# Performance work log

Hardware: AMD Instinct MI355X
Metric: run time of the kernel (lower is better)

## Reference

```python
import jax, jax.numpy as jnp
import numpy as np

T = 100          # sequence length (number of GRU steps)
H = 50           # carry/hidden dim
Z = 10           # latent dim
OUT = Z + Z * (Z + 1) // 2  # 65: mean + tril Cholesky entries
LN_EPS = 1e-6    # flax LayerNorm default epsilon


def setup_inputs() -> dict:
    key = jax.random.key(0)
    ks = jax.random.split(key, 8)
    # Orthogonal-ish recurrent kernels via QR for well-conditioned dynamics
    def ortho(k):
        a = jax.random.normal(k, (H, H), dtype=jnp.float32)
        q, _ = jnp.linalg.qr(a)
        return q
    return {
        "carry_init": jax.random.normal(ks[0], (H,), dtype=jnp.float32),
        "W_hr": ortho(ks[1]), "b_hr": jnp.zeros((H,), jnp.float32),
        "s_r": jnp.ones((H,), jnp.float32), "o_r": jnp.zeros((H,), jnp.float32),
        "W_hz": ortho(ks[2]), "b_hz": jnp.zeros((H,), jnp.float32),
        "s_z": jnp.ones((H,), jnp.float32), "o_z": jnp.zeros((H,), jnp.float32),
        "W_hn": ortho(ks[3]), "b_hn": jnp.zeros((H,), jnp.float32),
        "s_n": jnp.ones((H,), jnp.float32), "o_n": jnp.zeros((H,), jnp.float32),
        "W_dense": jax.random.normal(ks[4], (H, OUT), jnp.float32) * (1.0 / jnp.sqrt(H)),
        "b_dense": jnp.zeros((OUT,), jnp.float32),
    }


def _layernorm(x, scale, bias):
    mu = jnp.mean(x, axis=-1, keepdims=True)
    var = jnp.mean(jnp.square(x - mu), axis=-1, keepdims=True)
    return (x - mu) * jax.lax.rsqrt(var + LN_EPS) * scale + bias


def reference(carry_init, W_hr, b_hr, s_r, o_r, W_hz, b_hz, s_z, o_z,
              W_hn, b_hn, s_n, o_n, W_dense, b_dense):
    # Input to the GRU is zeros((T,1)) -> cell ignores it entirely (no input kernel).
    def step(h, _):
        r = jax.nn.sigmoid(_layernorm(h @ W_hr + b_hr, s_r, o_r))
        z = jax.nn.sigmoid(_layernorm(h @ W_hz + b_hz, s_z, o_z))
        n = jnp.tanh(r * _layernorm(h @ W_hn + b_hn, s_n, o_n))
        new_h = (1.0 - z) * n + z * h
        return new_h, new_h

    _, hs = jax.lax.scan(step, carry_init, None, length=T)  # (T, H)
    out = hs @ W_dense + b_dense                              # (T, OUT)

    tril = jnp.tril_indices(Z)
    eye = jnp.eye(Z, dtype=out.dtype)

    def nat(x):
        mu, flat = x[:Z], x[Z:]
        L = jnp.zeros((Z, Z), dtype=x.dtype).at[tril].set(flat)
        d = jax.nn.softplus(jnp.diagonal(L))  # positive diagonal -> PD Sigma
        L = L.at[jnp.diag_indices(Z)].set(d)
        Sigma = L @ L.T
        # psd_solve: J = Sigma^{-1} via Cholesky solve
        J = jax.scipy.linalg.cho_solve((L, True), eye)
        h_nat = J @ mu
        return Sigma, mu, J, h_nat

    Sigma, mu, J, h_nat = jax.vmap(nat)(out)
    return Sigma, mu, J, h_nat
```

## Files before the change

### kernel.cpp

```cpp
#include <hip/hip_runtime.h>
#include <hip/hip_bf16.h>
#include <math.h>

#define T_STEPS 100
#define H_DIM   50
#define Z_DIM   10
#define OUT_DIM 65
#define KP      25

typedef _Float16 half2v __attribute__((ext_vector_type(2)));

__device__ __forceinline__ float bcast_lane(float v, int lane) {
    return __uint_as_float(__builtin_amdgcn_readlane(__float_as_uint(v), lane));
}
__device__ __forceinline__ unsigned readlane_u(unsigned v, int lane) {
    return (unsigned)__builtin_amdgcn_readlane((int)v, lane);
}
template<int CTRL>
__device__ __forceinline__ float dpp_mov(float x) {
    return __uint_as_float((unsigned)__builtin_amdgcn_update_dpp(
        0, (int)__float_as_uint(x), CTRL, 0xF, 0xF, true));
}
#define DPP_ROW_SHL1 0x101
#define DPP_SHR1     0x111
#define DPP_SHR2     0x112
#define DPP_SHR4     0x114
#define DPP_SHR8     0x118
#define DPP_BCAST15  0x142
#define DPP_BCAST31  0x143

__device__ __forceinline__ unsigned pack_h2(float lo, float hi) {
#if __has_builtin(__builtin_amdgcn_cvt_pkrtz)
    return __builtin_bit_cast(unsigned, __builtin_amdgcn_cvt_pkrtz(lo, hi));
#else
    half2v p; p.x = (_Float16)lo; p.y = (_Float16)hi;
    return __builtin_bit_cast(unsigned, p);
#endif
}
__device__ __forceinline__ float fdot2h(unsigned a, unsigned b, float c) {
#if __has_builtin(__builtin_amdgcn_fdot2)
    return __builtin_amdgcn_fdot2(__builtin_bit_cast(half2v, a),
                                  __builtin_bit_cast(half2v, b), c, false);
#else
    const half2v x = __builtin_bit_cast(half2v, a);
    const half2v y = __builtin_bit_cast(half2v, b);
    return fmaf((float)x.x, (float)y.x, fmaf((float)x.y, (float)y.y, c));
#endif
}

__device__ __forceinline__ float fast_rcp(float x) { return __builtin_amdgcn_rcpf(x); }
__device__ __forceinline__ float fast_rsq(float x) { return __builtin_amdgcn_rsqf(x); }
__device__ __forceinline__ float fast_sigmoid(float x) {
    return fast_rcp(1.0f + __expf(-x));
}
__device__ __forceinline__ float fast_tanh(float y) {
    return 1.0f - 2.0f * fast_rcp(__expf(2.0f * y) + 1.0f);
}

__global__ __launch_bounds__(192, 1)
void gru_recur_kernel(
    const float* __restrict__ carry_init,
    const float* __restrict__ W_hr, const float* __restrict__ b_hr,
    const float* __restrict__ s_r,  const float* __restrict__ o_r,
    const float* __restrict__ W_hz, const float* __restrict__ b_hz,
    const float* __restrict__ s_z,  const float* __restrict__ o_z,
    const float* __restrict__ W_hn, const float* __restrict__ b_hn,
    const float* __restrict__ s_n,  const float* __restrict__ o_n,
    float* __restrict__ ws_h)
{
    const int  tid   = threadIdx.x;
    const int  wave  = tid >> 6;
    const int  j     = tid & 63;
    const bool valid = (j < H_DIM);
    const int  jc    = valid ? j : 0;

    const float* Wg = (wave == 0) ? W_hr : (wave == 1) ? W_hz : W_hn;
    const float* bg = (wave == 0) ? b_hr : (wave == 1) ? b_hz : b_hn;
    const float* sg = (wave == 0) ? s_r  : (wave == 1) ? s_z  : s_n;
    const float* og = (wave == 0) ? o_r  : (wave == 1) ? o_z  : o_n;

    unsigned w[KP];
    #pragma unroll
    for (int k = 0; k < KP; ++k) {
        const int i0 = 2 * k, i1 = 2 * k + 1;
        w[k] = pack_h2(valid ? Wg[i0 * H_DIM + j] : 0.0f,
                       valid ? Wg[i1 * H_DIM + j] : 0.0f);
    }
    #pragma unroll
    for (int k = 0; k < KP; ++k) asm volatile("" : "+v"(w[k]));

    const float bj = valid ? bg[jc] : 0.0f;
    const float sc = sg[jc];
    const float of = og[jc];

    __shared__ float gbuf[2][3][64];
    __shared__ __align__(16) float hist[T_STEPS][64];

    float h = valid ? carry_init[jc] : 0.0f;
    const float invH = 1.0f / (float)H_DIM;

    float    hsl = dpp_mov<DPP_ROW_SHL1>(h);
    unsigned hpk = pack_h2(h, hsl);

    #pragma unroll 1
    for (int t = 0; t < T_STEPS; ++t) {
        float a0 = bj, a1 = 0.0f;
        #pragma unroll
        for (int k = 0; k < KP; k += 2) {
            const unsigned s0 = readlane_u(hpk, 2 * k);
            a0 = fdot2h(s0, w[k], a0);
            if (k + 1 < KP) {
                const unsigned s1 = readlane_u(hpk, 2 * (k + 1));
                a1 = fdot2h(s1, w[k + 1], a1);
            }
        }
        const float a = a0 + a1;

        float m = a, q = a * a;
        #define STAGE(C) m += dpp_mov<C>(m); q += dpp_mov<C>(q);
        STAGE(DPP_SHR1) STAGE(DPP_SHR2) STAGE(DPP_SHR4)
        STAGE(DPP_SHR8) STAGE(DPP_BCAST15) STAGE(DPP_BCAST31)
        #undef STAGE
        m = bcast_lane(m, 63); q = bcast_lane(q, 63);

        const float mu  = m * invH;
        const float var = fmaxf(q * invH - mu * mu, 0.0f);
        const float g   = (a - mu) * fast_rsq(var + 1e-6f) * sc + of;
        const float val = (wave == 2) ? g : fast_sigmoid(g);

        gbuf[t & 1][wave][j] = val;
        __syncthreads();

        const float r  = gbuf[t & 1][0][j];
        const float z  = gbuf[t & 1][1][j];
        const float gn = gbuf[t & 1][2][j];
        const float n  = fast_tanh(r * gn);
        h = n + z * (h - n);

        if (wave == 0) hist[t][j] = h;

        hsl = dpp_mov<DPP_ROW_SHL1>(h);
        hpk = pack_h2(h, hsl);
    }

    __syncthreads();
    {
        float4*       dst = (float4*)ws_h;
        const float4* src = (const float4*)hist;
        for (int i = tid; i < T_STEPS * 16; i += 192)
            dst[i] = src[i];
    }
}

__global__ __launch_bounds__(128)
void dense_nat_kernel(
    const float* __restrict__ W_dense, const float* __restrict__ b_dense,
    const float* __restrict__ ws_h, float* __restrict__ out)
{
    const int t   = blockIdx.x;
    const int tid = threadIdx.x;

    __shared__ float hloc[H_DIM];
    __shared__ float dl  [OUT_DIM];
    __shared__ float Lp  [55];
    __shared__ float Li  [55];
    __shared__ float Jsh [100];

    if (tid < H_DIM) hloc[tid] = ws_h[t * 64 + tid];
    __syncthreads();

    if (tid < OUT_DIM) {
        float acc = b_dense[tid];
        #pragma unroll
        for (int i = 0; i < H_DIM; ++i)
            acc = fmaf(hloc[i], W_dense[i * OUT_DIM + tid], acc);
        dl[tid] = acc;
    }
    __syncthreads();

    if (tid < 55) {
        float v = dl[Z_DIM + tid];
        const bool isd = (tid==0)|(tid==2)|(tid==5)|(tid==9)|(tid==14)|
                         (tid==20)|(tid==27)|(tid==35)|(tid==44)|(tid==54);
        if (isd) v = (v > 20.0f) ? v : log1pf(__expf(v));
        Lp[tid] = v;
    }
    __syncthreads();

    float* outSigma = out;
    float* outMu    = out + 10000;
    float* outJ     = out + 11000;
    float* outHnat  = out + 21000;

    int a = 0;
    {
        #pragma unroll
        for (int x = 1; x < Z_DIM; ++x)
            if (tid >= x * (x + 1) / 2) a = x;
    }
    const int b = tid - a * (a + 1) / 2;

    if (tid < 55) {
        float s = 0.0f;
        for (int k = 0; k <= b; ++k)
            s = fmaf(Lp[a * (a + 1) / 2 + k], Lp[b * (b + 1) / 2 + k], s);
        outSigma[t * 100 + a * 10 + b] = s;
        outSigma[t * 100 + b * 10 + a] = s;
    }
    if (tid >= 64 && tid < 64 + Z_DIM) outMu[t * 10 + (tid - 64)] = dl[tid - 64];
    __syncthreads();

    if (tid < Z_DIM) {
        const int k = tid;
        float dinv[Z_DIM];
        #pragma unroll
        for (int i = 0; i < Z_DIM; ++i)
            dinv[i] = 1.0f / Lp[i * (i + 1) / 2 + i];
        float col[Z_DIM];
        #pragma unroll
        for (int i = 0; i < Z_DIM; ++i) col[i] = 0.0f;
        #pragma unroll
        for (int i = 0; i < Z_DIM; ++i) {
            float s = 0.0f;
            #pragma unroll
            for (int m = 0; m < i; ++m)
                s = fmaf(Lp[i * (i + 1) / 2 + m], col[m], s);
            if (i >= k) col[i] = (i == k) ? dinv[i] : -s * dinv[i];
        }
        #pragma unroll
        for (int i = 0; i < Z_DIM; ++i)
            if (i >= k) Li[i * (i + 1) / 2 + k] = col[i];
    }
    __syncthreads();

    if (tid < 55) {
        float s = 0.0f;
        for (int m = a; m < Z_DIM; ++m)
            s = fmaf(Li[m * (m + 1) / 2 + a], Li[m * (m + 1) / 2 + b], s);
        outJ[t * 100 + a * 10 + b] = s;
        outJ[t * 100 + b * 10 + a] = s;
        Jsh[a * 10 + b] = s;
        Jsh[b * 10 + a] = s;
    }
    __syncthreads();

    if (tid < Z_DIM) {
        float s = 0.0f;
        #pragma unroll
        for (int k = 0; k < Z_DIM; ++k)
            s = fmaf(Jsh[tid * 10 + k], dl[k], s);
        outHnat[t * 10 + tid] = s;
    }
}

extern "C" void kernel_launch(void* const* d_in, const int* in_sizes, int n_in,
                              void* d_out, int out_size, void* d_ws, size_t ws_size,
                              hipStream_t stream) {
    const float* p[15];
    for (int i = 0; i < 15; ++i) p[i] = (const float*)d_in[i];
    float* ws_h = (float*)d_ws;

    gru_recur_kernel<<<dim3(1), dim3(192), 0, stream>>>(
        p[0],
        p[1], p[2], p[3], p[4],
        p[5], p[6], p[7], p[8],
        p[9], p[10], p[11], p[12],
        ws_h);

    dense_nat_kernel<<<dim3(T_STEPS), dim3(128), 0, stream>>>(
        p[13], p[14], ws_h, (float*)d_out);
}
```

Before: 128.4 us.

## Fuse dense/natural-param stage into GRU kernel with pipelined consumer waves

Merges the recurrence and the per-timestep dense projection plus Cholesky inverse into one single-block kernel. Two extra waves process timestep t-1 while the three GRU waves compute step t, alternating timesteps between them and reading hidden states directly from shared memory. This removes the second kernel launch and the workspace round trip, hiding the post-processing behind the serial recurrence. In exchange, every step's block barrier now includes two more waves, and their work can delay the critical path if it exceeds two step durations.

Result: slower. 446.6 us (+247.7%).

```diff
diff --git a/kernel.cpp b/kernel.cpp
--- a/kernel.cpp
+++ b/kernel.cpp
@@ -57,8 +57,12 @@
     return 1.0f - 2.0f * fast_rcp(__expf(2.0f * y) + 1.0f);
 }
 
-__global__ __launch_bounds__(192, 1)
-void gru_recur_kernel(
+__device__ __forceinline__ void lds_fence_wave() {
+    asm volatile("s_waitcnt lgkmcnt(0)" ::: "memory");
+}
+
+__global__ __launch_bounds__(320, 1)
+void gru_fused_kernel(
     const float* __restrict__ carry_init,
     const float* __restrict__ W_hr, const float* __restrict__ b_hr,
     const float* __restrict__ s_r,  const float* __restrict__ o_r,
@@ -66,190 +70,195 @@
     const float* __restrict__ s_z,  const float* __restrict__ o_z,
     const float* __restrict__ W_hn, const float* __restrict__ b_hn,
     const float* __restrict__ s_n,  const float* __restrict__ o_n,
-    float* __restrict__ ws_h)
+    const float* __restrict__ W_dense, const float* __restrict__ b_dense,
+    float* __restrict__ out)
 {
-    const int  tid   = threadIdx.x;
-    const int  wave  = tid >> 6;
-    const int  j     = tid & 63;
-    const bool valid = (j < H_DIM);
-    const int  jc    = valid ? j : 0;
-
-    const float* Wg = (wave == 0) ? W_hr : (wave == 1) ? W_hz : W_hn;
-    const float* bg = (wave == 0) ? b_hr : (wave == 1) ? b_hz : b_hn;
-    const float* sg = (wave == 0) ? s_r  : (wave == 1) ? s_z  : s_n;
-    const float* og = (wave == 0) ? o_r  : (wave == 1) ? o_z  : o_n;
-
-    unsigned w[KP];
-    #pragma unroll
-    for (int k = 0; k < KP; ++k) {
-        const int i0 = 2 * k, i1 = 2 * k + 1;
-        w[k] = pack_h2(valid ? Wg[i0 * H_DIM + j] : 0.0f,
-                       valid ? Wg[i1 * H_DIM + j] : 0.0f);
-    }
-    #pragma unroll
-    for (int k = 0; k < KP; ++k) asm volatile("" : "+v"(w[k]));
-
-    const float bj = valid ? bg[jc] : 0.0f;
-    const float sc = sg[jc];
-    const float of = og[jc];
+    const int tid  = threadIdx.x;
+    const int wave = tid >> 6;
+    const int j    = tid & 63;
 
     __shared__ float gbuf[2][3][64];
     __shared__ __align__(16) float hist[T_STEPS][64];
-
-    float h = valid ? carry_init[jc] : 0.0f;
-    const float invH = 1.0f / (float)H_DIM;
-
-    float    hsl = dpp_mov<DPP_ROW_SHL1>(h);
-    unsigned hpk = pack_h2(h, hsl);
-
-    #pragma unroll 1
-    for (int t = 0; t < T_STEPS; ++t) {
-        float a0 = bj, a1 = 0.0f;
+    __shared__ float Lp[2][56];
+    __shared__ float Li[2][56];
+    __shared__ float Jsh[2][100];
+    __shared__ float mrow[2][12];
+
+    if (wave < 3) {
+        const bool valid = (j < H_DIM);
+        const int  jc    = valid ? j : 0;
+
+        const float* Wg = (wave == 0) ? W_hr : (wave == 1) ? W_hz : W_hn;
+        const float* bg = (wave == 0) ? b_hr : (wave == 1) ? b_hz : b_hn;
+        const float* sg = (wave == 0) ? s_r  : (wave == 1) ? s_z  : s_n;
+        const float* og = (wave == 0) ? o_r  : (wave == 1) ? o_z  : o_n;
+
+        unsigned w[KP];
         #pragma unroll
-        for (int k = 0; k < KP; k += 2) {
-            const unsigned s0 = readlane_u(hpk, 2 * k);
-            a0 = fdot2h(s0, w[k], a0);
-            if (k + 1 < KP) {
-                const unsigned s1 = readlane_u(hpk, 2 * (k + 1));
-                a1 = fdot2h(s1, w[k + 1], a1);
-            }
+        for (int k = 0; k < KP; ++k) {
+            const int i0 = 2 * k, i1 = 2 * k + 1;
+            w[k] = pack_h2(valid ? Wg[i0 * H_DIM + j] : 0.0f,
+                           valid ? Wg[i1 * H_DIM + j] : 0.0f);
         }
-        const float a = a0 + a1;
-
-        float m = a, q = a * a;
-        #define STAGE(C) m += dpp_mov<C>(m); q += dpp_mov<C>(q);
-        STAGE(DPP_SHR1) STAGE(DPP_SHR2) STAGE(DPP_SHR4)
-        STAGE(DPP_SHR8) STAGE(DPP_BCAST15) STAGE(DPP_BCAST31)
-        #undef STAGE
-        m = bcast_lane(m, 63); q = bcast_lane(q, 63);
-
-        const float mu  = m * invH;
-        const float var = fmaxf(q * invH - mu * mu, 0.0f);
-        const float g   = (a - mu) * fast_rsq(var + 1e-6f) * sc + of;
-        const float val = (wave == 2) ? g : fast_sigmoid(g);
-
-        gbuf[t & 1][wave][j] = val;
+        #pragma unroll
+        for (int k = 0; k < KP; ++k) asm volatile("" : "+v"(w[k]));
+
+        const float bj = valid ? bg[jc] : 0.0f;
+        const float sc = sg[jc];
+        const float of = og[jc];
+
+        float h = valid ? carry_init[jc] : 0.0f;
+        const float invH = 1.0f / (float)H_DIM;
+
+        float    hsl = dpp_mov<DPP_ROW_SHL1>(h);
+        unsigned hpk = pack_h2(h, hsl);
+
+        #pragma unroll 1
+        for (int t = 0; t < T_STEPS; ++t) {
+            float a0 = bj, a1 = 0.0f;
+            #pragma unroll
+            for (int k = 0; k < KP; k += 2) {
+                const unsigned s0 = readlane_u(hpk, 2 * k);
+                a0 = fdot2h(s0, w[k], a0);
+                if (k + 1 < KP) {
+                    const unsigned s1 = readlane_u(hpk, 2 * (k + 1));
+                    a1 = fdot2h(s1, w[k + 1], a1);
+                }
+            }
+            const float a = a0 + a1;
+
+            float m = a, q = a * a;
+            #define STAGE(C) m += dpp_mov<C>(m); q += dpp_mov<C>(q);
+            STAGE(DPP_SHR1) STAGE(DPP_SHR2) STAGE(DPP_SHR4)
+            STAGE(DPP_SHR8) STAGE(DPP_BCAST15) STAGE(DPP_BCAST31)
+            #undef STAGE
+            m = bcast_lane(m, 63); q = bcast_lane(q, 63);
+
+            const float mu  = m * invH;
+            const float var = fmaxf(q * invH - mu * mu, 0.0f);
+            const float g   = (a - mu) * fast_rsq(var + 1e-6f) * sc + of;
+            const float val = (wave == 2) ? g : fast_sigmoid(g);
+
+            gbuf[t & 1][wave][j] = val;
+            __syncthreads();
+
+            const float r  = gbuf[t & 1][0][j];
+            const float z  = gbuf[t & 1][1][j];
+            const float gn = gbuf[t & 1][2][j];
+            const float n  = fast_tanh(r * gn);
+            h = n + z * (h - n);
+
+            if (wave == 0) hist[t][j] = h;
+
+            hsl = dpp_mov<DPP_ROW_SHL1>(h);
+            hpk = pack_h2(h, hsl);
+        }
         __syncthreads();
-
-        const float r  = gbuf[t & 1][0][j];
-        const float z  = gbuf[t & 1][1][j];
-        const float gn = gbuf[t & 1][2][j];
-        const float n  = fast_tanh(r * gn);
-        h = n + z * (h - n);
-
-        if (wave == 0) hist[t][j] = h;
-
-        hsl = dpp_mov<DPP_ROW_SHL1>(h);
-        hpk = pack_h2(h, hsl);
-    }
-
-    __syncthreads();
-    {
-        float4*       dst = (float4*)ws_h;
-        const float4* src = (const float4*)hist;
-        for (int i = tid; i < T_STEPS * 16; i += 192)
-            dst[i] = src[i];
-    }
-}
-
-__global__ __launch_bounds__(128)
-void dense_nat_kernel(
-    const float* __restrict__ W_dense, const float* __restrict__ b_dense,
-    const float* __restrict__ ws_h, float* __restrict__ out)
-{
-    const int t   = blockIdx.x;
-    const int tid = threadIdx.x;
-
-    __shared__ float hloc[H_DIM];
-    __shared__ float dl  [OUT_DIM];
-    __shared__ float Lp  [55];
-    __shared__ float Li  [55];
-    __shared__ float Jsh [100];
-
-    if (tid < H_DIM) hloc[tid] = ws_h[t * 64 + tid];
-    __syncthreads();
-
-    if (tid < OUT_DIM) {
-        float acc = b_dense[tid];
-        #pragma unroll
-        for (int i = 0; i < H_DIM; ++i)
-            acc = fmaf(hloc[i], W_dense[i * OUT_DIM + tid], acc);
-        dl[tid] = acc;
-    }
-    __syncthreads();
-
-    if (tid < 55) {
-        float v = dl[Z_DIM + tid];
-        const bool isd = (tid==0)|(tid==2)|(tid==5)|(tid==9)|(tid==14)|
-                         (tid==20)|(tid==27)|(tid==35)|(tid==44)|(tid==54);
-        if (isd) v = (v > 20.0f) ? v : log1pf(__expf(v));
-        Lp[tid] = v;
-    }
-    __syncthreads();
-
-    float* outSigma = out;
-    float* outMu    = out + 10000;
-    float* outJ     = out + 11000;
-    float* outHnat  = out + 21000;
-
-    int a = 0;
-    {
+    } else {
+        const int dw = wave - 3;
+        int a = 0;
         #pragma unroll
         for (int x = 1; x < Z_DIM; ++x)
-            if (tid >= x * (x + 1) / 2) a = x;
-    }
-    const int b = tid - a * (a + 1) / 2;
-
-    if (tid < 55) {
-        float s = 0.0f;
-        for (int k = 0; k <= b; ++k)
-            s = fmaf(Lp[a * (a + 1) / 2 + k], Lp[b * (b + 1) / 2 + k], s);
-        outSigma[t * 100 + a * 10 + b] = s;
-        outSigma[t * 100 + b * 10 + a] = s;
-    }
-    if (tid >= 64 && tid < 64 + Z_DIM) outMu[t * 10 + (tid - 64)] = dl[tid - 64];
-    __syncthreads();
-
-    if (tid < Z_DIM) {
-        const int k = tid;
-        float dinv[Z_DIM];
-        #pragma unroll
-        for (int i = 0; i < Z_DIM; ++i)
-            dinv[i] = 1.0f / Lp[i * (i + 1) / 2 + i];
-        float col[Z_DIM];
-        #pragma unroll
-        for (int i = 0; i < Z_DIM; ++i) col[i] = 0.0f;
-        #pragma unroll
-        for (int i = 0; i < Z_DIM; ++i) {
-            float s = 0.0f;
+            if (j >= x * (x + 1) / 2) a = x;
+        const int b   = j - a * (a + 1) / 2;
+        const int col = (j < 55) ? (10 + j) : (j - 55);
+        const float bdp = b_dense[col];
+        const float bd9 = (j == 0) ? b_dense[9] : 0.0f;
+        const bool isd = (j==0)|(j==2)|(j==5)|(j==9)|(j==14)|
+                         (j==20)|(j==27)|(j==35)|(j==44)|(j==54);
+
+        float* outSigma = out;
+        float* outMu    = out + 10000;
+        float* outJ     = out + 11000;
+        float* outHnat  = out + 21000;
+
+        auto dense_step = [&](int s) {
+            float acc = bdp, acc9 = bd9;
             #pragma unroll
-            for (int m = 0; m < i; ++m)
-                s = fmaf(Lp[i * (i + 1) / 2 + m], col[m], s);
-            if (i >= k) col[i] = (i == k) ? dinv[i] : -s * dinv[i];
+            for (int i = 0; i < H_DIM; ++i) {
+                const float hi = hist[s][i];
+                acc = fmaf(hi, W_dense[i * OUT_DIM + col], acc);
+            }
+            if (j == 0) {
+                #pragma unroll
+                for (int i = 0; i < H_DIM; ++i)
+                    acc9 = fmaf(hist[s][i], W_dense[i * OUT_DIM + 9], acc9);
+            }
+
+            if (j < 55) {
+                float v = acc;
+                if (isd) v = (v > 20.0f) ? v : log1pf(__expf(v));
+                Lp[dw][j] = v;
+            } else {
+                mrow[dw][j - 55] = acc;
+            }
+            if (j == 0) mrow[dw][9] = acc9;
+            lds_fence_wave();
+
+            if (j < 55) {
+                float sgm = 0.0f;
+                for (int k = 0; k <= b; ++k)
+                    sgm = fmaf(Lp[dw][a * (a + 1) / 2 + k],
+                               Lp[dw][b * (b + 1) / 2 + k], sgm);
+                outSigma[s * 100 + a * 10 + b] = sgm;
+                outSigma[s * 100 + b * 10 + a] = sgm;
+            } else {
+                outMu[s * 10 + (j - 55)] = acc;
+            }
+            if (j == 0) outMu[s * 10 + 9] = acc9;
+
+            if (j < Z_DIM) {
+                const int k = j;
+                float dinv[Z_DIM];
+                #pragma unroll
+                for (int i = 0; i < Z_DIM; ++i)
+                    dinv[i] = 1.0f / Lp[dw][i * (i + 1) / 2 + i];
+                float c[Z_DIM];
+                #pragma unroll
+                for (int i = 0; i < Z_DIM; ++i) c[i] = 0.0f;
+                #pragma unroll
+                for (int i = 0; i < Z_DIM; ++i) {
+                    float sfs = 0.0f;
+                    #pragma unroll
+                    for (int m = 0; m < i; ++m)
+                        sfs = fmaf(Lp[dw][i * (i + 1) / 2 + m], c[m], sfs);
+                    if (i >= k) c[i] = (i == k) ? dinv[i] : -sfs * dinv[i];
+                }
+                #pragma unroll
+                for (int i = 0; i < Z_DIM; ++i)
+                    if (i >= k) Li[dw][i * (i + 1) / 2 + k] = c[i];
+            }
+            lds_fence_wave();
+
+            if (j < 55) {
+                float sj = 0.0f;
+                for (int m = a; m < Z_DIM; ++m)
+                    sj = fmaf(Li[dw][m * (m + 1) / 2 + a],
+                              Li[dw][m * (m + 1) / 2 + b], sj);
+                outJ[s * 100 + a * 10 + b] = sj;
+                outJ[s * 100 + b * 10 + a] = sj;
+                Jsh[dw][a * 10 + b] = sj;
+                Jsh[dw][b * 10 + a] = sj;
+            }
+            lds_fence_wave();
+
+            if (j < Z_DIM) {
+                float sh = 0.0f;
+                #pragma unroll
+                for (int k2 = 0; k2 < Z_DIM; ++k2)
+                    sh = fmaf(Jsh[dw][j * 10 + k2], mrow[dw][k2], sh);
+                outHnat[s * 10 + j] = sh;
+            }
+        };
+
+        #pragma unroll 1
+        for (int t = 0; t < T_STEPS; ++t) {
+            __syncthreads();
+            const int s = t - 1;
+            if (s >= 0 && (s & 1) == dw) dense_step(s);
         }
-        #pragma unroll
-        for (int i = 0; i < Z_DIM; ++i)
-            if (i >= k) Li[i * (i + 1) / 2 + k] = col[i];
-    }
-    __syncthreads();
-
-    if (tid < 55) {
-        float s = 0.0f;
-        for (int m = a; m < Z_DIM; ++m)
-            s = fmaf(Li[m * (m + 1) / 2 + a], Li[m * (m + 1) / 2 + b], s);
-        outJ[t * 100 + a * 10 + b] = s;
-        outJ[t * 100 + b * 10 + a] = s;
-        Jsh[a * 10 + b] = s;
-        Jsh[b * 10 + a] = s;
-    }
-    __syncthreads();
-
-    if (tid < Z_DIM) {
-        float s = 0.0f;
-        #pragma unroll
-        for (int k = 0; k < Z_DIM; ++k)
-            s = fmaf(Jsh[tid * 10 + k], dl[k], s);
-        outHnat[t * 10 + tid] = s;
+        __syncthreads();
+        if (dw == 1) dense_step(T_STEPS - 1);
     }
 }
 
@@ -258,15 +267,12 @@
                               hipStream_t stream) {
     const float* p[15];
     for (int i = 0; i < 15; ++i) p[i] = (const float*)d_in[i];
-    float* ws_h = (float*)d_ws;
-
-    gru_recur_kernel<<<dim3(1), dim3(192), 0, stream>>>(
+
+    gru_fused_kernel<<<dim3(1), dim3(320), 0, stream>>>(
         p[0],
         p[1], p[2], p[3], p[4],
         p[5], p[6], p[7], p[8],
         p[9], p[10], p[11], p[12],
-        ws_h);
-
-    dense_nat_kernel<<<dim3(T_STEPS), dim3(128), 0, stream>>>(
-        p[13], p[14], ws_h, (float*)d_out);
-}
+        p[13], p[14],
+        (float*)d_out);
+}
```
